# Kernel optimization log

Hardware: AMD Instinct MI355X
Metric: run time of the kernel (lower is better)

The kernel has to match this reference:

```python
import jax, jax.numpy as jnp
import numpy as np

MARGIN = 1.0   # TripletLoss(margin) init arg
EPS = 1e-6     # torch F.pairwise_distance eps used by nn.TripletMarginLoss
INF = 1e9

N, D_EMB, N_CLASSES = 8192, 1024, 128


def setup_inputs() -> dict:
    key = jax.random.key(0)
    k1, k2 = jax.random.split(key)
    embeddings = jax.random.normal(k1, (N, D_EMB), dtype=jnp.float32)
    target = jax.random.randint(k2, (N,), 0, N_CLASSES, dtype=jnp.int64 if jax.config.jax_enable_x64 else jnp.int32)
    return {"embeddings": embeddings, "target": target}


def _mine_and_loss(embeddings, target):
    # Vectorized, deterministic equivalent of the per-anchor random mining loop:
    # full pairwise L2 distance matrix via a GEMM (compute-bound core).
    sq = jnp.sum(embeddings * embeddings, axis=1)                      # [N]
    d2 = sq[:, None] + sq[None, :] - 2.0 * (embeddings @ embeddings.T)  # [N, N]
    Dm = jnp.sqrt(jnp.maximum(d2, 0.0))                                 # [N, N]

    same = target[:, None] == target[None, :]
    eye = jnp.eye(target.shape[0], dtype=bool)
    pos_mask = same & ~eye          # valid positives (same class, not self)
    neg_mask = ~same                # valid negatives (different class)

    # Positive: hardest (farthest) same-class sample (deterministic stand-in
    # for the original's random positive draw).
    pos_scores = jnp.where(pos_mask, Dm, -INF)
    pos_idx = jnp.argmax(pos_scores, axis=1)                           # [N]
    d_p = jnp.max(pos_scores, axis=1)                                  # [N]

    # Negative: semi-hard (d_p < d_n < d_p + margin), pick the closest such
    # negative; if none exists, fall back to the overall hardest (min-dist)
    # negative -- mirrors the loop's early-break vs. min_dist fallback.
    semi = neg_mask & (Dm > d_p[:, None]) & (Dm < (d_p + MARGIN)[:, None])
    has_semi = jnp.any(semi, axis=1)
    neg_semi = jnp.argmin(jnp.where(semi, Dm, INF), axis=1)
    neg_hard = jnp.argmin(jnp.where(neg_mask, Dm, INF), axis=1)
    neg_idx = jnp.where(has_semi, neg_semi, neg_hard)                  # [N]

    # nn.TripletMarginLoss(margin, p=2): mean(relu(d(a,p) - d(a,n) + margin))
    # with torch's pairwise_distance eps added to the difference.
    a = embeddings
    p = embeddings[pos_idx]
    n = embeddings[neg_idx]
    dp = jnp.sqrt(jnp.sum((a - p + EPS) ** 2, axis=1))
    dn = jnp.sqrt(jnp.sum((a - n + EPS) ** 2, axis=1))
    return jnp.mean(jax.nn.relu(dp - dn + MARGIN))


def reference(embeddings, target):
    return _mine_and_loss(embeddings, target)
```

## Files before the change

kernel.cpp:

```cpp
#include <hip/hip_runtime.h>
#include <hip/hip_bf16.h>

#define N 8192
#define D 1024
#define MARGIN 1.0f
#define EPS 1e-6f

typedef __attribute__((ext_vector_type(8))) short bf16x8;
typedef __attribute__((ext_vector_type(4))) float f32x4;
typedef __attribute__((ext_vector_type(8))) _Float16 f16x8;
typedef __attribute__((ext_vector_type(4))) _Float16 f16x4;
typedef __attribute__((ext_vector_type(8))) unsigned short u16x8;

__device__ inline unsigned short f2bf(float x) {
    unsigned u = __float_as_uint(x);
    unsigned r = (u + 0x7FFFu + ((u >> 16) & 1u)) >> 16;
    return (unsigned short)r;
}

__device__ inline float h2f(unsigned hb) {
    return (float)__builtin_bit_cast(_Float16, (unsigned short)hb);
}

__global__ __launch_bounds__(256) void prep_kernel(const float* __restrict__ E,
                                                   unsigned short* __restrict__ Ebf,
                                                   float* __restrict__ sq) {
    const int r = blockIdx.x;
    const int tid = threadIdx.x;
    const float4 v = ((const float4*)(E + (size_t)r * D))[tid];
    ushort4 o;
    o.x = f2bf(v.x); o.y = f2bf(v.y); o.z = f2bf(v.z); o.w = f2bf(v.w);
    ((ushort4*)(Ebf + (size_t)r * D))[tid] = o;
    float s = v.x * v.x + v.y * v.y + v.z * v.z + v.w * v.w;
    for (int off = 32; off > 0; off >>= 1) s += __shfl_down(s, off);
    __shared__ float red[4];
    const int lane = tid & 63, wave = tid >> 6;
    if (lane == 0) red[wave] = s;
    __syncthreads();
    if (tid == 0) sq[r] = red[0] + red[1] + red[2] + red[3];
}

__global__ __launch_bounds__(256) void cls_kernel(const int* __restrict__ target,
                                                  unsigned char* __restrict__ cls) {
    const int t = blockIdx.x * 256 + threadIdx.x;
    cls[t] = (unsigned char)target[t];
}


#define SLOT_0A0 0
#define SLOT_0A1 16384
#define SLOT_0B0 32768
#define SLOT_0B1 49152
#define SLOT_1A0 65536
#define SLOT_1A1 81920
#define SLOT_1B0 98304
#define SLOT_1B1 114688

#define STAGE(slotOff, baseRow, kcol) do {                                              \
    const unsigned short* _s0 = E + (size_t)((baseRow) + (tid >> 2)) * D + (kcol) + stc * 8; \
    __builtin_amdgcn_global_load_lds(                                                    \
        (const __attribute__((address_space(1))) unsigned int*)_s0,                      \
        (__attribute__((address_space(3))) unsigned int*)(smem + (slotOff) + wave * 1024), 16, 0, 0); \
    const unsigned short* _s1 = _s0 + (size_t)128 * D;                                   \
    __builtin_amdgcn_global_load_lds(                                                    \
        (const __attribute__((address_space(1))) unsigned int*)_s1,                      \
        (__attribute__((address_space(3))) unsigned int*)(smem + (slotOff) + 8192 + wave * 1024), 16, 0, 0); \
} while (0)

#define PHASE(b, ks, mq, LOADB, SLOT_ST, TILE_ST, BASE_ST, KH_ST, DO_VM) do {            \
    const char* _As = smem + (b) * 65536 + (ks) * 16384;                                 \
    const char* _Bs = smem + (b) * 65536 + 32768 + (ks) * 16384;                         \
    if (LOADB) {                                                                         \
        _Pragma("unroll") for (int nj = 0; nj < 4; ++nj)                                 \
            bfr[nj] = *(const bf16x8*)(_Bs + (wn * 64 + nj * 16 + mr) * 64 + swz);       \
    }                                                                                    \
    bf16x8 af[4];                                                                        \
    _Pragma("unroll") for (int mi = 0; mi < 4; ++mi)                                     \
        af[mi] = *(const bf16x8*)(_As + (wm * 128 + (mq) * 64 + mi * 16 + mr) * 64 + swz); \
    STAGE(SLOT_ST, BASE_ST, (TILE_ST) * 64 + (KH_ST));                                   \
    __asm__ __volatile__("s_barrier" ::: "memory");                                      \
    __builtin_amdgcn_s_setprio(1);                                                       \
    _Pragma("unroll") for (int mi = 0; mi < 4; ++mi)                                     \
        _Pragma("unroll") for (int nj = 0; nj < 4; ++nj)                                 \
            acc[(mq) * 4 + mi][nj] = __builtin_amdgcn_mfma_f32_16x16x32_bf16(            \
                af[mi], bfr[nj], acc[(mq) * 4 + mi][nj], 0, 0, 0);                       \
    __builtin_amdgcn_s_setprio(0);                                                       \
    if (DO_VM) __asm__ __volatile__("s_waitcnt vmcnt(6)" ::: "memory");                  \
    __asm__ __volatile__("s_barrier" ::: "memory");                                      \
} while (0)

__global__ __launch_bounds__(512, 2) void gemm_kernel(const unsigned short* __restrict__ E,
                                                      const float* __restrict__ sq,
                                                      _Float16* __restrict__ D2h) {
    extern __shared__ char smem[];

    const int tid = threadIdx.x;
    const int lane = tid & 63;
    const int wave = tid >> 6;
    const int wm = wave >> 2;
    const int wn = wave & 3;
    const int mr = lane & 15;
    const int q = lane >> 4;
    const int swz = ((q ^ ((mr >> 1) & 3)) << 4);
    const int stc = (tid & 3) ^ ((tid >> 3) & 3);

    const int l = blockIdx.x;
    int by = (int)((sqrtf(8.0f * (float)l + 1.0f) - 1.0f) * 0.5f);
    while ((by + 1) * (by + 2) / 2 <= l) ++by;
    while (by * (by + 1) / 2 > l) --by;
    const int bx = l - by * (by + 1) / 2;
    const int rm = by * 256;
    const int cn = bx * 256;

    f32x4 acc[8][4] = {};
    bf16x8 bfr[4];

    STAGE(SLOT_0A0, rm, 0);
    STAGE(SLOT_0B0, cn, 0);
    STAGE(SLOT_0A1, rm, 32);
    STAGE(SLOT_0B1, cn, 32);
    STAGE(SLOT_1A0, rm, 64);
    __asm__ __volatile__("s_waitcnt vmcnt(6)" ::: "memory");
    __asm__ __volatile__("s_barrier" ::: "memory");

    for (int i = 0; i < 8; ++i) {
        const int kt = 2 * i;
        const int t2 = (kt + 2 < 16) ? kt + 2 : 15;
        const int t3 = (kt + 3 < 16) ? kt + 3 : 15;
        PHASE(0, 0, 0, 1, SLOT_1B0, kt + 1, cn, 0, 0);
        PHASE(0, 0, 1, 0, SLOT_1A1, kt + 1, rm, 32, 1);
        PHASE(0, 1, 0, 1, SLOT_1B1, kt + 1, cn, 32, 0);
        PHASE(0, 1, 1, 0, SLOT_0A0, t2, rm, 0, 1);
        PHASE(1, 0, 0, 1, SLOT_0B0, t2, cn, 0, 0);
        PHASE(1, 0, 1, 0, SLOT_0A1, t2, rm, 32, 1);
        PHASE(1, 1, 0, 1, SLOT_0B1, t2, cn, 32, 0);
        PHASE(1, 1, 1, 0, SLOT_1A0, t3, rm, 0, 1);
    }

    const int crow = q * 4;
    float sqj[4];
#pragma unroll
    for (int nj = 0; nj < 4; ++nj) sqj[nj] = sq[cn + wn * 64 + nj * 16 + mr];
    const bool offd = (bx != by);
#pragma unroll
    for (int mg = 0; mg < 8; ++mg) {
        const int i0 = rm + wm * 128 + mg * 16 + crow;
        const f32x4 sqi = *(const f32x4*)(sq + i0);
#pragma unroll
        for (int nj = 0; nj < 4; ++nj) {
            const int j = cn + wn * 64 + nj * 16 + mr;
            f16x4 tv;
#pragma unroll
            for (int r = 0; r < 4; ++r) {
                const float d2 = fmaxf(sqi[r] + sqj[nj] - 2.0f * acc[mg][nj][r], 0.0f);
                const _Float16 h = (_Float16)d2;
                tv[r] = h;
                D2h[(size_t)(i0 + r) * N + j] = h;
            }
            if (offd) *(f16x4*)(D2h + (size_t)j * N + i0) = tv;
        }
    }
}

__global__ __launch_bounds__(256) void mine_kernel(const _Float16* __restrict__ D2h,
                                                   const unsigned char* __restrict__ cls,
                                                   float* __restrict__ loss_arr) {
    const int i = blockIdx.x;
    const int tid = threadIdx.x;
    const int lane = tid & 63, wave = tid >> 6;
    const unsigned tcb = cls[i];
    const unsigned short* row = (const unsigned short*)(D2h + (size_t)i * N);

    u16x8 v[4];
    unsigned long long c8[4];
#pragma unroll
    for (int it = 0; it < 4; ++it) {
        v[it] = *(const u16x8*)(row + it * 2048 + tid * 8);
        c8[it] = *(const unsigned long long*)(cls + it * 2048 + tid * 8);
    }

    unsigned pm = 0u, nm = 0xFFFFu;
#pragma unroll
    for (int it = 0; it < 4; ++it) {
#pragma unroll
        for (int e = 0; e < 8; ++e) {
            const unsigned hb = v[it][e];
            const bool s = ((unsigned)(c8[it] >> (8 * e)) & 0xFFu) == tcb;
            pm = max(pm, s ? hb : 0u);
            nm = min(nm, s ? 0xFFFFu : hb);
        }
    }
    for (int off = 1; off < 64; off <<= 1) {
        pm = max(pm, (unsigned)__shfl_xor((int)pm, off));
        nm = min(nm, (unsigned)__shfl_xor((int)nm, off));
    }
    __shared__ unsigned redp[4], redn[4], reds[4];
    if (lane == 0) { redp[wave] = pm; redn[wave] = nm; }
    __syncthreads();
    pm = max(max(redp[0], redp[1]), max(redp[2], redp[3]));
    nm = min(min(redn[0], redn[1]), min(redn[2], redn[3]));
    const unsigned lob = pm;

    unsigned sm = 0xFFFFu;
#pragma unroll
    for (int it = 0; it < 4; ++it) {
#pragma unroll
        for (int e = 0; e < 8; ++e) {
            const unsigned hb = v[it][e];
            sm = min(sm, hb > lob ? hb : 0xFFFFu);
        }
    }
    for (int off = 1; off < 64; off <<= 1)
        sm = min(sm, (unsigned)__shfl_xor((int)sm, off));
    if (lane == 0) reds[wave] = sm;
    __syncthreads();
    if (tid == 0) {
        sm = min(min(reds[0], reds[1]), min(reds[2], reds[3]));
        const float lo = h2f(lob);
        const float dp = sqrtf(lo);
        const float hw = dp + MARGIN;
        const float hi = hw * hw;
        const float smv = h2f(sm);
        const float dn2 = (smv < hi) ? smv : h2f(nm);
        loss_arr[i] = fmaxf(dp - sqrtf(dn2) + MARGIN, 0.0f);
    }
}

__global__ __launch_bounds__(256) void reduce_kernel(const float* __restrict__ loss_arr,
                                                     float* __restrict__ out) {
    const int tid = threadIdx.x;
    float s = 0.0f;
    for (int k = tid; k < N; k += 256) s += loss_arr[k];
    for (int off = 32; off > 0; off >>= 1) s += __shfl_down(s, off);
    __shared__ float red[4];
    const int lane = tid & 63, wave = tid >> 6;
    if (lane == 0) red[wave] = s;
    __syncthreads();
    if (tid == 0) out[0] = (red[0] + red[1] + red[2] + red[3]) * (1.0f / N);
}

extern "C" void kernel_launch(void* const* d_in, const int* in_sizes, int n_in,
                              void* d_out, int out_size, void* d_ws, size_t ws_size,
                              hipStream_t stream) {
    const float* E = (const float*)d_in[0];
    const int* target = (const int*)d_in[1];
    float* out = (float*)d_out;
    char* ws = (char*)d_ws;

    unsigned short* Ebf = (unsigned short*)ws;
    float* sq        = (float*)(ws + (size_t)16777216);
    float* loss_arr  = (float*)(ws + (size_t)16809984);
    unsigned char* cls = (unsigned char*)(ws + (size_t)16842752);
    _Float16* D2h    = (_Float16*)(ws + (size_t)16875520);

    static bool attr_set = false;
    if (!attr_set) {
        hipFuncSetAttribute((const void*)gemm_kernel,
                            hipFuncAttributeMaxDynamicSharedMemorySize, 131072);
        attr_set = true;
    }

    prep_kernel<<<N, 256, 0, stream>>>(E, Ebf, sq);
    cls_kernel<<<N / 256, 256, 0, stream>>>(target, cls);
    gemm_kernel<<<528, 512, 131072, stream>>>(Ebf, sq, D2h);
    mine_kernel<<<N, 256, 0, stream>>>(D2h, cls, loss_arr);
    reduce_kernel<<<1, 256, 0, stream>>>(loss_arr, out);
}
```

Before: 215.5 us.

## Split diagonal GEMM tiles into separate kernel and swizzle off-diagonal tile order

After: 216.3 us. No clear change (+0.4%).

```diff
diff --git a/kernel.cpp b/kernel.cpp
--- a/kernel.cpp
+++ b/kernel.cpp
@@ -78,7 +78,6 @@
     _Pragma("unroll") for (int mi = 0; mi < 4; ++mi)                                     \
         af[mi] = *(const bf16x8*)(_As + (wm * 128 + (mq) * 64 + mi * 16 + mr) * 64 + swz); \
     STAGE(SLOT_ST, BASE_ST, (TILE_ST) * 64 + (KH_ST));                                   \
-    __asm__ __volatile__("s_barrier" ::: "memory");                                      \
     __builtin_amdgcn_s_setprio(1);                                                       \
     _Pragma("unroll") for (int mi = 0; mi < 4; ++mi)                                     \
         _Pragma("unroll") for (int nj = 0; nj < 4; ++nj)                                 \
@@ -104,11 +103,13 @@
     const int swz = ((q ^ ((mr >> 1) & 3)) << 4);
     const int stc = (tid & 3) ^ ((tid >> 3) & 3);
 
-    const int l = blockIdx.x;
-    int by = (int)((sqrtf(8.0f * (float)l + 1.0f) - 1.0f) * 0.5f);
-    while ((by + 1) * (by + 2) / 2 <= l) ++by;
-    while (by * (by + 1) / 2 > l) --by;
-    const int bx = l - by * (by + 1) / 2;
+    const int h = blockIdx.x;
+    const int l = (h & 7) * 62 + (h >> 3);
+
+    int by = (int)((1.0f + sqrtf(8.0f * (float)l + 1.0f)) * 0.5f);
+    while (by * (by - 1) / 2 > l) --by;
+    while ((by + 1) * by / 2 <= l) ++by;
+    const int bx = l - by * (by - 1) / 2;
     const int rm = by * 256;
     const int cn = bx * 256;
 
@@ -141,7 +142,6 @@
     float sqj[4];
 #pragma unroll
     for (int nj = 0; nj < 4; ++nj) sqj[nj] = sq[cn + wn * 64 + nj * 16 + mr];
-    const bool offd = (bx != by);
 #pragma unroll
     for (int mg = 0; mg < 8; ++mg) {
         const int i0 = rm + wm * 128 + mg * 16 + crow;
@@ -153,11 +153,114 @@
 #pragma unroll
             for (int r = 0; r < 4; ++r) {
                 const float d2 = fmaxf(sqi[r] + sqj[nj] - 2.0f * acc[mg][nj][r], 0.0f);
-                const _Float16 h = (_Float16)d2;
+                const _Float16 h16 = (_Float16)d2;
+                tv[r] = h16;
+                D2h[(size_t)(i0 + r) * N + j] = h16;
+            }
+            *(f16x4*)(D2h + (size_t)j * N + i0) = tv;
+        }
+    }
+}
+
+__global__ __launch_bounds__(256) void gemm_diag_kernel(const unsigned short* __restrict__ E,
+                                                        const float* __restrict__ sq,
+                                                        _Float16* __restrict__ D2h) {
+    __shared__ char smem[128 * 136 * 2];
+    unsigned short* As = (unsigned short*)smem;
+    unsigned short* Bs = (unsigned short*)(smem + 8192);
+    _Float16* Ts = (_Float16*)smem;
+
+    const int tid = threadIdx.x;
+    const int lane = tid & 63;
+    const int wave = tid >> 6;
+    const int wm = wave & 1, wn = wave >> 1;
+
+    const int c = blockIdx.x;
+    const int t = c / 3, s = c - 3 * t;
+    const int sm = (s + 1) >> 1;
+    const int sn = s >> 1;
+    const int rm = t * 256 + sm * 128;
+    const int cn = t * 256 + sn * 128;
+    const bool offdiag = (s == 1);
+
+    const int srow = tid >> 2;
+    const int scol = (tid & 3) * 8;
+
+    const unsigned short* gA = E + (size_t)(rm + srow) * D + scol;
+    const unsigned short* gB = E + (size_t)(cn + srow) * D + scol;
+
+    f32x4 acc[4][4] = {};
+
+    const int kq = (lane >> 4) * 8;
+    const int mr = lane & 15;
+
+    for (int k0 = 0; k0 < D; k0 += 32) {
+        __builtin_amdgcn_global_load_lds(
+            (const __attribute__((address_space(1))) unsigned int*)(gA + k0),
+            (__attribute__((address_space(3))) unsigned int*)((char*)As + wave * 1024), 16, 0, 0);
+        __builtin_amdgcn_global_load_lds(
+            (const __attribute__((address_space(1))) unsigned int*)(gA + (size_t)64 * D + k0),
+            (__attribute__((address_space(3))) unsigned int*)((char*)As + 4096 + wave * 1024), 16, 0, 0);
+        __builtin_amdgcn_global_load_lds(
+            (const __attribute__((address_space(1))) unsigned int*)(gB + k0),
+            (__attribute__((address_space(3))) unsigned int*)((char*)Bs + wave * 1024), 16, 0, 0);
+        __builtin_amdgcn_global_load_lds(
+            (const __attribute__((address_space(1))) unsigned int*)(gB + (size_t)64 * D + k0),
+            (__attribute__((address_space(3))) unsigned int*)((char*)Bs + 4096 + wave * 1024), 16, 0, 0);
+        __syncthreads();
+
+        bf16x8 af[4], bfr[4];
+#pragma unroll
+        for (int mi = 0; mi < 4; ++mi)
+            af[mi] = *(const bf16x8*)(As + (wm * 64 + mi * 16 + mr) * 32 + kq);
+#pragma unroll
+        for (int ni = 0; ni < 4; ++ni)
+            bfr[ni] = *(const bf16x8*)(Bs + (wn * 64 + ni * 16 + mr) * 32 + kq);
+#pragma unroll
+        for (int mi = 0; mi < 4; ++mi)
+#pragma unroll
+            for (int ni = 0; ni < 4; ++ni)
+                acc[mi][ni] = __builtin_amdgcn_mfma_f32_16x16x32_bf16(af[mi], bfr[ni], acc[mi][ni], 0, 0, 0);
+        __syncthreads();
+    }
+
+    const int crow = (lane >> 4) * 4;
+    const int ccol = lane & 15;
+    float sqj[4];
+#pragma unroll
+    for (int ni = 0; ni < 4; ++ni)
+        sqj[ni] = sq[cn + wn * 64 + ni * 16 + ccol];
+#pragma unroll
+    for (int mi = 0; mi < 4; ++mi) {
+        const int lrow = wm * 64 + mi * 16 + crow;
+        const int i0 = rm + lrow;
+        float sqi[4];
+#pragma unroll
+        for (int r = 0; r < 4; ++r) sqi[r] = sq[i0 + r];
+#pragma unroll
+        for (int ni = 0; ni < 4; ++ni) {
+            const int lcol = wn * 64 + ni * 16 + ccol;
+            const int j = cn + lcol;
+            f16x4 tv;
+#pragma unroll
+            for (int r = 0; r < 4; ++r) {
+                float d2 = fmaxf(sqi[r] + sqj[ni] - 2.0f * acc[mi][ni][r], 0.0f);
+                _Float16 h = (_Float16)d2;
+                D2h[(size_t)(i0 + r) * N + j] = h;
                 tv[r] = h;
-                D2h[(size_t)(i0 + r) * N + j] = h;
             }
-            if (offd) *(f16x4*)(D2h + (size_t)j * N + i0) = tv;
+            if (offdiag)
+                *(f16x4*)(Ts + (size_t)lcol * 136 + lrow) = tv;
+        }
+    }
+    if (offdiag) {
+        __syncthreads();
+#pragma unroll
+        for (int it = 0; it < 8; ++it) {
+            const int rt = it * 16 + (tid >> 4);
+            const int seg = tid & 15;
+            f16x8 v = *(const f16x8*)(Ts + (size_t)rt * 136 + seg * 8);
+            *(f16x8*)(D2h + (size_t)(cn + rt) * N + rm + seg * 8) = v;
         }
     }
 }
@@ -262,7 +365,8 @@
 
     prep_kernel<<<N, 256, 0, stream>>>(E, Ebf, sq);
     cls_kernel<<<N / 256, 256, 0, stream>>>(target, cls);
-    gemm_kernel<<<528, 512, 131072, stream>>>(Ebf, sq, D2h);
+    gemm_kernel<<<496, 512, 131072, stream>>>(Ebf, sq, D2h);
+    gemm_diag_kernel<<<96, 256, 0, stream>>>(Ebf, sq, D2h);
     mine_kernel<<<N, 256, 0, stream>>>(D2h, cls, loss_arr);
     reduce_kernel<<<1, 256, 0, stream>>>(loss_arr, out);
 }
```
